# Kernel optimization log

Measured on AMD Instinct MI355X. Metric: run time of the kernel, lower is better.

The kernel has to match this reference:

```python
import jax, jax.numpy as jnp
import numpy as np

BETA = 0.9
THRESHOLD = 1.0


def setup_inputs() -> dict:
    key = jax.random.key(0)
    k1, k2 = jax.random.split(key)
    T, N_IN, N_OUT = 1024, 4096, 4096
    x = jax.random.normal(k1, (T, N_IN), dtype=jnp.float32)
    # fc1 weight initialized uniform[0,1), shape [out, in] like nn.Linear
    W = jax.random.uniform(k2, (N_OUT, N_IN), dtype=jnp.float32)
    return {"x": x, "W": W}


def reference(x, W):
    # Precompute the batched linear projection over all timesteps: [T, N_OUT]
    cur = jnp.einsum('ti,oi->to', x, W)
    mem0 = jnp.zeros((W.shape[0],), dtype=x.dtype)

    def step(mem, c):
        # snntorch Leaky, reset_mechanism='subtract':
        # reset is computed from the PREVIOUS membrane potential (detached)
        reset = (mem > THRESHOLD).astype(mem.dtype)
        mem_new = BETA * mem + c - reset * THRESHOLD
        spk = (mem_new > THRESHOLD).astype(mem.dtype)
        return mem_new, (spk, mem_new)

    _, (spk_rec, mem_rec) = jax.lax.scan(step, mem0, cur)
    return spk_rec, mem_rec
```

## Files before the change

### kernel.cpp

```cpp
#include <hip/hip_runtime.h>
#include <hip/hip_bf16.h>
#include <stdint.h>


typedef __attribute__((ext_vector_type(8))) short bf16x8;
typedef __attribute__((ext_vector_type(4))) float floatx4;

#define T_STEPS 1024
#define N_IN    4096
#define N_OUT   4096

#define PH_T 128
#define NPH  (T_STEPS / PH_T)
#define NB_N 16
#define TP   130

#define TN ((size_t)T_STEPS * N_OUT)

__device__ __forceinline__ unsigned short f2bf_rne(float f) {
    unsigned int u = __builtin_bit_cast(unsigned int, f);
    unsigned int r = 0x7FFFu + ((u >> 16) & 1u);
    return (unsigned short)((u + r) >> 16);
}

__device__ __forceinline__ float bf2f(unsigned short b) {
    unsigned int u = ((unsigned int)b) << 16;
    return __builtin_bit_cast(float, u);
}

__global__ __launch_bounds__(256) void cvt2_kernel(const float4* __restrict__ inX,
                                                   ushort4* __restrict__ outX, int n4x,
                                                   const float4* __restrict__ inW,
                                                   ushort4* __restrict__ outW, int n4w) {
    int i = blockIdx.x * blockDim.x + threadIdx.x;
    const float4* in;
    ushort4* out;
    int k;
    if (i < n4x) { in = inX; out = outX; k = i; }
    else         { in = inW; out = outW; k = i - n4x; if (k >= n4w) return; }
    float4 v = in[k];
    ushort4 o;
    o.x = f2bf_rne(v.x);
    o.y = f2bf_rne(v.y);
    o.z = f2bf_rne(v.z);
    o.w = f2bf_rne(v.w);
    out[k] = o;
}

__device__ __forceinline__ void gload16(const void* g, void* l) {
    __builtin_amdgcn_global_load_lds((const __attribute__((address_space(1))) void*)g,
                                     (__attribute__((address_space(3))) void*)l,
                                     16, 0, 0);
}

#define SB0()  __builtin_amdgcn_sched_barrier(0)
#define BARR() __builtin_amdgcn_s_barrier()

__global__ __launch_bounds__(512, 2) void gemm8(const short* __restrict__ A,
                                                const short* __restrict__ B,
                                                unsigned short* __restrict__ Pb,
                                                int kLen) {
    __shared__ short lds[65536];

    const int tid  = threadIdx.x;
    const int lane = tid & 63;
    const int wv   = tid >> 6;
    const int wm   = (wv >> 2) * 128;
    const int wn   = (wv & 3) * 64;

    const int bid  = blockIdx.x;
    const int z    = bid >> 6;
    const int tile = bid & 63;
    const long bm  = (long)(tile >> 4) * 256;
    const long bn  = (long)(tile & 15) * 256;
    const int kBeg = z * kLen;
    unsigned short* __restrict__ Pz = Pb + (size_t)z * TN;
    const int NT    = kLen / 64;
    const int NITER = NT / 2;

    const int srow = lane >> 3;
    const int scol = ((lane & 7) ^ srow) << 3;
    const short* aSrc = A + (bm + wv * 8 + srow) * (long)N_IN + kBeg + scol;
    const short* bSrc = B + (bn + wv * 8 + srow) * (long)N_IN + kBeg + scol;
    const int ldA = wv * 512;
    const int ldB = 32768 + wv * 512;

    const int fm    = lane & 15;
    const int fko   = (lane >> 4) * 8;
    const int cbase = fko ^ ((fm & 7) << 3);

    floatx4 acc[8][4] = {};
    bf16x8 af[4][2];
    bf16x8 bq[2][2][2];

    auto loadA = [&](int b, int qm) {
#pragma unroll
        for (int mi = 0; mi < 4; ++mi)
#pragma unroll
            for (int ks = 0; ks < 2; ++ks)
                af[mi][ks] = *(const bf16x8*)(
                    lds + b * 16384 + (wm + qm * 64 + mi * 16 + fm) * 64 +
                    (cbase ^ (ks << 5)));
    };
    auto loadB = [&](int b, int qn) {
#pragma unroll
        for (int nj = 0; nj < 2; ++nj)
#pragma unroll
            for (int ks = 0; ks < 2; ++ks)
                bq[qn][nj][ks] = *(const bf16x8*)(
                    lds + 32768 + b * 16384 + (wn + qn * 32 + nj * 16 + fm) * 64 +
                    (cbase ^ (ks << 5)));
    };
    auto mfma16 = [&](int qm, int qn) {
        __builtin_amdgcn_s_setprio(1);
#pragma unroll
        for (int ks = 0; ks < 2; ++ks)
#pragma unroll
            for (int mi = 0; mi < 4; ++mi)
#pragma unroll
                for (int nj = 0; nj < 2; ++nj)
                    acc[qm * 4 + mi][qn * 2 + nj] =
                        __builtin_amdgcn_mfma_f32_16x16x32_bf16(
                            af[mi][ks], bq[qn][nj][ks],
                            acc[qm * 4 + mi][qn * 2 + nj], 0, 0, 0);
        __builtin_amdgcn_s_setprio(0);
    };
    auto stageA = [&](int b, int h, int t) {
        const short* s = aSrc + (size_t)(h * 128) * N_IN + t * 64;
        gload16(s,                    lds + b * 16384 + h * 8192 + ldA);
        gload16(s + (size_t)64 * N_IN, lds + b * 16384 + h * 8192 + 4096 + ldA);
    };
    auto stageB = [&](int b, int h, int t) {
        const short* s = bSrc + (size_t)(h * 128) * N_IN + t * 64;
        gload16(s,                    lds + b * 16384 + h * 8192 + ldB);
        gload16(s + (size_t)64 * N_IN, lds + b * 16384 + h * 8192 + 4096 + ldB);
    };

    stageA(0, 0, 0); stageA(0, 1, 0);
    stageB(0, 0, 0); stageB(0, 1, 0);
    stageB(1, 0, 1); stageB(1, 1, 1);
    asm volatile("s_waitcnt vmcnt(4)" ::: "memory");
    SB0();
    BARR();

    for (int i = 0; i < NITER; ++i) {
        const int t1 = 2 * i + 1;
        const int t2 = 2 * i + 2;
        const int t3 = 2 * i + 3;
        const bool more = (i + 1 < NITER);

        loadA(0, 0); loadB(0, 0);
        stageA(1, 0, t1);
        asm volatile("s_waitcnt lgkmcnt(8)" ::: "memory");
        SB0(); BARR();
        asm volatile("s_waitcnt lgkmcnt(0)" ::: "memory"); SB0();
        mfma16(0, 0);
        SB0(); BARR();

        loadB(0, 1);
        stageA(1, 1, t1);
        SB0(); BARR();
        asm volatile("s_waitcnt lgkmcnt(0)" ::: "memory"); SB0();
        mfma16(0, 1);
        SB0(); BARR();

        loadA(0, 1);
        if (more) stageB(0, 0, t2);
        SB0(); BARR();
        asm volatile("s_waitcnt lgkmcnt(0)" ::: "memory"); SB0();
        mfma16(1, 0);
        SB0(); BARR();

        if (more) stageB(0, 1, t2);
        SB0(); BARR();
        mfma16(1, 1);
        if (more) { asm volatile("s_waitcnt vmcnt(4)" ::: "memory"); }
        else      { asm volatile("s_waitcnt vmcnt(0)" ::: "memory"); }
        SB0(); BARR();

        loadA(1, 0); loadB(1, 0);
        if (more) stageA(0, 0, t2);
        asm volatile("s_waitcnt lgkmcnt(8)" ::: "memory");
        SB0(); BARR();
        asm volatile("s_waitcnt lgkmcnt(0)" ::: "memory"); SB0();
        mfma16(0, 0);
        SB0(); BARR();

        loadB(1, 1);
        if (more) stageA(0, 1, t2);
        SB0(); BARR();
        asm volatile("s_waitcnt lgkmcnt(0)" ::: "memory"); SB0();
        mfma16(0, 1);
        SB0(); BARR();

        loadA(1, 1);
        if (more) stageB(1, 0, t3);
        SB0(); BARR();
        asm volatile("s_waitcnt lgkmcnt(0)" ::: "memory"); SB0();
        mfma16(1, 0);
        SB0(); BARR();

        if (more) stageB(1, 1, t3);
        SB0(); BARR();
        mfma16(1, 1);
        if (more) { asm volatile("s_waitcnt vmcnt(4)" ::: "memory"); }
        SB0(); BARR();
    }

    const int cn = lane & 15;
    const int cm = (lane >> 4) * 4;
#pragma unroll
    for (int mi = 0; mi < 8; ++mi)
#pragma unroll
        for (int nj = 0; nj < 4; ++nj)
#pragma unroll
            for (int r = 0; r < 4; ++r)
                Pz[(bm + wm + mi * 16 + cm + r) * (long)N_OUT + bn + wn + nj * 16 + cn] =
                    f2bf_rne(acc[mi][nj][r]);
}

template <int NPART>
__global__ __launch_bounds__(512) void scan_kernel(const unsigned short* __restrict__ Pb,
                                                   float* __restrict__ out) {
    __shared__ float ringCur[2][NB_N * TP];
    __shared__ float ringMem[2][NB_N * TP];

    const int tid  = threadIdx.x;
    const int wv   = tid >> 6;
    const int lane = tid & 63;
    const int n0   = blockIdx.x * NB_N;

    const int pn = lane & 15;
    const int tr = lane >> 4;

    float mem = 0.0f;

    if (wv < 7) {
        float v[NPART][5];
        int gi[5];
#pragma unroll
        for (int i = 0; i < 5; ++i) {
            int g = wv + 7 * i;
            gi[i] = g;
            if (g < 32) {
                size_t idx = (size_t)(g * 4 + tr) * N_OUT + n0 + pn;
#pragma unroll
                for (int zz = 0; zz < NPART; ++zz)
                    v[zz][i] = bf2f(Pb[(size_t)zz * TN + idx]);
            }
        }
#pragma unroll
        for (int i = 0; i < 5; ++i)
            if (gi[i] < 32) {
                float s = v[0][i];
#pragma unroll
                for (int zz = 1; zz < NPART; ++zz) s += v[zz][i];
                ringCur[0][pn * TP + gi[i] * 4 + tr] = s;
            }
    }
    __syncthreads();

    for (int ph = 0; ph < NPH; ++ph) {
        if (wv < 7) {
            if (ph >= 1) {
                const float* mr = ringMem[(ph - 1) & 1];
                const size_t tb = (size_t)(ph - 1) * PH_T;
                float mv[5];
                int gi[5];
#pragma unroll
                for (int i = 0; i < 5; ++i) {
                    int g = wv + 7 * i;
                    gi[i] = g;
                    if (g < 32) mv[i] = mr[pn * TP + g * 4 + tr];
                }
#pragma unroll
                for (int i = 0; i < 5; ++i)
                    if (gi[i] < 32) {
                        size_t idx = (tb + gi[i] * 4 + tr) * N_OUT + n0 + pn;
                        out[idx]      = mv[i] > 1.0f ? 1.0f : 0.0f;
                        out[TN + idx] = mv[i];
                    }
            }
            if (ph + 1 < NPH) {
                const size_t tb = (size_t)(ph + 1) * PH_T;
                float v[NPART][5];
                int gi[5];
#pragma unroll
                for (int i = 0; i < 5; ++i) {
                    int g = wv + 7 * i;
                    gi[i] = g;
                    if (g < 32) {
                        size_t idx = (tb + g * 4 + tr) * N_OUT + n0 + pn;
#pragma unroll
                        for (int zz = 0; zz < NPART; ++zz)
                            v[zz][i] = bf2f(Pb[(size_t)zz * TN + idx]);
                    }
                }
#pragma unroll
                for (int i = 0; i < 5; ++i)
                    if (gi[i] < 32) {
                        float s = v[0][i];
#pragma unroll
                        for (int zz = 1; zz < NPART; ++zz) s += v[zz][i];
                        ringCur[(ph + 1) & 1][pn * TP + gi[i] * 4 + tr] = s;
                    }
            }
        } else if (lane < 16) {
            const float* base = &ringCur[ph & 1][pn * TP];
            float* mbase = &ringMem[ph & 1][pn * TP];
#pragma unroll
            for (int sub = 0; sub < 4; ++sub) {
                float2 buf[16];
#pragma unroll
                for (int q = 0; q < 16; ++q)
                    buf[q] = *(const float2*)&base[sub * 32 + q * 2];
#pragma unroll
                for (int q = 0; q < 16; ++q) {
                    float rst = mem > 1.0f ? 1.0f : 0.0f;
                    mem = fmaf(0.9f, mem, buf[q].x) - rst;
                    float m0 = mem;
                    rst = mem > 1.0f ? 1.0f : 0.0f;
                    mem = fmaf(0.9f, mem, buf[q].y) - rst;
                    float2 mo; mo.x = m0; mo.y = mem;
                    *(float2*)&mbase[sub * 32 + q * 2] = mo;
                }
            }
        }
        __syncthreads();
    }

    if (wv < 7) {
        const float* mr = ringMem[(NPH - 1) & 1];
        const size_t tb = (size_t)(NPH - 1) * PH_T;
        float mv[5];
        int gi[5];
#pragma unroll
        for (int i = 0; i < 5; ++i) {
            int g = wv + 7 * i;
            gi[i] = g;
            if (g < 32) mv[i] = mr[pn * TP + g * 4 + tr];
        }
#pragma unroll
        for (int i = 0; i < 5; ++i)
            if (gi[i] < 32) {
                size_t idx = (tb + gi[i] * 4 + tr) * N_OUT + n0 + pn;
                out[idx]      = mv[i] > 1.0f ? 1.0f : 0.0f;
                out[TN + idx] = mv[i];
            }
    }
}

extern "C" void kernel_launch(void* const* d_in, const int* in_sizes, int n_in,
                              void* d_out, int out_size, void* d_ws, size_t ws_size,
                              hipStream_t stream) {
    const float* x = (const float*)d_in[0];
    const float* W = (const float*)d_in[1];
    float* out = (float*)d_out;

    char* ws = (char*)d_ws;
    const size_t xbBytes = (size_t)T_STEPS * N_IN * 2;
    const size_t WbBytes = (size_t)N_OUT * N_IN * 2;
    const size_t PBytes  = TN * 2;
    short* xb = (short*)ws;
    short* Wb = (short*)(ws + xbBytes);
    unsigned short* Pb = (unsigned short*)(ws + xbBytes + WbBytes);

    int S = 1;
    if (ws_size >= xbBytes + WbBytes + 4 * PBytes)      S = 4;
    else if (ws_size >= xbBytes + WbBytes + 2 * PBytes) S = 2;

    {
        const int n4x = T_STEPS * N_IN / 4;
        const int n4w = N_OUT * N_IN / 4;
        const int nthr = n4x + n4w;
        cvt2_kernel<<<(nthr + 255) / 256, 256, 0, stream>>>(
            (const float4*)x, (ushort4*)xb, n4x,
            (const float4*)W, (ushort4*)Wb, n4w);
    }

    gemm8<<<64 * S, 512, 0, stream>>>(xb, Wb, Pb, N_IN / S);

    if (S == 4)      scan_kernel<4><<<N_OUT / NB_N, 512, 0, stream>>>(Pb, out);
    else if (S == 2) scan_kernel<2><<<N_OUT / NB_N, 512, 0, stream>>>(Pb, out);
    else             scan_kernel<1><<<N_OUT / NB_N, 512, 0, stream>>>(Pb, out);
}
```

Baseline: 180.4 us.

## Store GEMM output transposed and vectorize scan staging and output writes

The GEMM epilogue now packs four bf16 results into a uint2 and writes the projection in neuron-major [N_OUT][T] layout, which gives contiguous 8-byte stores. The scan kernel then reads 8 contiguous timesteps per thread with 16-byte loads across the split-K partials, and writes spike and membrane outputs as float4. TP padding changes from 130 to 132 so the float4 LDS accesses stay aligned. The aim is to replace scattered 2-byte global loads and 4-byte stores with wide coalesced accesses, at the risk of LDS bank conflicts in the transposed writeOut reads.

```diff
diff --git a/kernel.cpp b/kernel.cpp
--- a/kernel.cpp
+++ b/kernel.cpp
@@ -13,7 +13,7 @@
 #define PH_T 128
 #define NPH  (T_STEPS / PH_T)
 #define NB_N 16
-#define TP   130
+#define TP   132
 
 #define TN ((size_t)T_STEPS * N_OUT)
 
@@ -212,11 +212,15 @@
 #pragma unroll
     for (int mi = 0; mi < 8; ++mi)
 #pragma unroll
-        for (int nj = 0; nj < 4; ++nj)
-#pragma unroll
-            for (int r = 0; r < 4; ++r)
-                Pz[(bm + wm + mi * 16 + cm + r) * (long)N_OUT + bn + wn + nj * 16 + cn] =
-                    f2bf_rne(acc[mi][nj][r]);
+        for (int nj = 0; nj < 4; ++nj) {
+            unsigned int lo = (unsigned int)f2bf_rne(acc[mi][nj][0]) |
+                              ((unsigned int)f2bf_rne(acc[mi][nj][1]) << 16);
+            unsigned int hi = (unsigned int)f2bf_rne(acc[mi][nj][2]) |
+                              ((unsigned int)f2bf_rne(acc[mi][nj][3]) << 16);
+            uint2 v; v.x = lo; v.y = hi;
+            size_t nIdx = (size_t)(bn + wn + nj * 16 + cn);
+            *(uint2*)(Pz + nIdx * T_STEPS + (size_t)(bm + wm + mi * 16 + cm)) = v;
+        }
 }
 
 template <int NPART>
@@ -231,80 +235,66 @@
     const int n0   = blockIdx.x * NB_N;
 
     const int pn = lane & 15;
-    const int tr = lane >> 4;
+
+    const int sn = tid >> 4;
+    const int sc = tid & 15;
 
     float mem = 0.0f;
 
-    if (wv < 7) {
-        float v[NPART][5];
-        int gi[5];
-#pragma unroll
-        for (int i = 0; i < 5; ++i) {
-            int g = wv + 7 * i;
-            gi[i] = g;
-            if (g < 32) {
-                size_t idx = (size_t)(g * 4 + tr) * N_OUT + n0 + pn;
-#pragma unroll
-                for (int zz = 0; zz < NPART; ++zz)
-                    v[zz][i] = bf2f(Pb[(size_t)zz * TN + idx]);
-            }
+    auto stage = [&](int buf, size_t tb) {
+        float s[8];
+#pragma unroll
+        for (int j = 0; j < 8; ++j) s[j] = 0.0f;
+#pragma unroll
+        for (int zz = 0; zz < NPART; ++zz) {
+            const uint4 v = *(const uint4*)(Pb + (size_t)zz * TN +
+                                            (size_t)(n0 + sn) * T_STEPS + tb + sc * 8);
+            unsigned int w0 = v.x, w1 = v.y, w2 = v.z, w3 = v.w;
+            s[0] += __builtin_bit_cast(float, w0 << 16);
+            s[1] += __builtin_bit_cast(float, w0 & 0xFFFF0000u);
+            s[2] += __builtin_bit_cast(float, w1 << 16);
+            s[3] += __builtin_bit_cast(float, w1 & 0xFFFF0000u);
+            s[4] += __builtin_bit_cast(float, w2 << 16);
+            s[5] += __builtin_bit_cast(float, w2 & 0xFFFF0000u);
+            s[6] += __builtin_bit_cast(float, w3 << 16);
+            s[7] += __builtin_bit_cast(float, w3 & 0xFFFF0000u);
         }
-#pragma unroll
-        for (int i = 0; i < 5; ++i)
-            if (gi[i] < 32) {
-                float s = v[0][i];
-#pragma unroll
-                for (int zz = 1; zz < NPART; ++zz) s += v[zz][i];
-                ringCur[0][pn * TP + gi[i] * 4 + tr] = s;
-            }
-    }
+        float4 f0; f0.x = s[0]; f0.y = s[1]; f0.z = s[2]; f0.w = s[3];
+        float4 f1; f1.x = s[4]; f1.y = s[5]; f1.z = s[6]; f1.w = s[7];
+        float* rc = &ringCur[buf][sn * TP + sc * 8];
+        *(float4*)rc = f0;
+        *(float4*)(rc + 4) = f1;
+    };
+
+    auto writeOut = [&](int buf, size_t tb) {
+        const float* mr = ringMem[buf];
+        for (int it = tid; it < 512; it += 448) {
+            int t  = it >> 2;
+            int nq = it & 3;
+            float m0 = mr[(nq * 4 + 0) * TP + t];
+            float m1 = mr[(nq * 4 + 1) * TP + t];
+            float m2 = mr[(nq * 4 + 2) * TP + t];
+            float m3 = mr[(nq * 4 + 3) * TP + t];
+            float4 mv; mv.x = m0; mv.y = m1; mv.z = m2; mv.w = m3;
+            float4 sv;
+            sv.x = m0 > 1.0f ? 1.0f : 0.0f;
+            sv.y = m1 > 1.0f ? 1.0f : 0.0f;
+            sv.z = m2 > 1.0f ? 1.0f : 0.0f;
+            sv.w = m3 > 1.0f ? 1.0f : 0.0f;
+            size_t idx = (tb + t) * N_OUT + n0 + nq * 4;
+            *(float4*)&out[idx]      = sv;
+            *(float4*)&out[TN + idx] = mv;
+        }
+    };
+
+    if (tid < 256) stage(0, 0);
     __syncthreads();
 
     for (int ph = 0; ph < NPH; ++ph) {
         if (wv < 7) {
-            if (ph >= 1) {
-                const float* mr = ringMem[(ph - 1) & 1];
-                const size_t tb = (size_t)(ph - 1) * PH_T;
-                float mv[5];
-                int gi[5];
-#pragma unroll
-                for (int i = 0; i < 5; ++i) {
-                    int g = wv + 7 * i;
-                    gi[i] = g;
-                    if (g < 32) mv[i] = mr[pn * TP + g * 4 + tr];
-                }
-#pragma unroll
-                for (int i = 0; i < 5; ++i)
-                    if (gi[i] < 32) {
-                        size_t idx = (tb + gi[i] * 4 + tr) * N_OUT + n0 + pn;
-                        out[idx]      = mv[i] > 1.0f ? 1.0f : 0.0f;
-                        out[TN + idx] = mv[i];
-                    }
-            }
-            if (ph + 1 < NPH) {
-                const size_t tb = (size_t)(ph + 1) * PH_T;
-                float v[NPART][5];
-                int gi[5];
-#pragma unroll
-                for (int i = 0; i < 5; ++i) {
-                    int g = wv + 7 * i;
-                    gi[i] = g;
-                    if (g < 32) {
-                        size_t idx = (tb + g * 4 + tr) * N_OUT + n0 + pn;
-#pragma unroll
-                        for (int zz = 0; zz < NPART; ++zz)
-                            v[zz][i] = bf2f(Pb[(size_t)zz * TN + idx]);
-                    }
-                }
-#pragma unroll
-                for (int i = 0; i < 5; ++i)
-                    if (gi[i] < 32) {
-                        float s = v[0][i];
-#pragma unroll
-                        for (int zz = 1; zz < NPART; ++zz) s += v[zz][i];
-                        ringCur[(ph + 1) & 1][pn * TP + gi[i] * 4 + tr] = s;
-                    }
-            }
+            if (ph >= 1) writeOut((ph - 1) & 1, (size_t)(ph - 1) * PH_T);
+            if (tid < 256 && ph + 1 < NPH)
+                stage((ph + 1) & 1, (size_t)(ph + 1) * PH_T);
         } else if (lane < 16) {
             const float* base = &ringCur[ph & 1][pn * TP];
             float* mbase = &ringMem[ph & 1][pn * TP];
@@ -329,25 +319,7 @@
         __syncthreads();
     }
 
-    if (wv < 7) {
-        const float* mr = ringMem[(NPH - 1) & 1];
-        const size_t tb = (size_t)(NPH - 1) * PH_T;
-        float mv[5];
-        int gi[5];
-#pragma unroll
-        for (int i = 0; i < 5; ++i) {
-            int g = wv + 7 * i;
-            gi[i] = g;
-            if (g < 32) mv[i] = mr[pn * TP + g * 4 + tr];
-        }
-#pragma unroll
-        for (int i = 0; i < 5; ++i)
-            if (gi[i] < 32) {
-                size_t idx = (tb + gi[i] * 4 + tr) * N_OUT + n0 + pn;
-                out[idx]      = mv[i] > 1.0f ? 1.0f : 0.0f;
-                out[TN + idx] = mv[i];
-            }
-    }
+    if (wv < 7) writeOut((NPH - 1) & 1, (size_t)(NPH - 1) * PH_T);
 }
 
 extern "C" void kernel_launch(void* const* d_in, const int* in_sizes, int n_in,
```

New measurement: 169.6 us. 1.06x faster.
